# Kernel optimization log

Hardware: AMD Instinct MI355X
Metric: run time of the kernel (lower is better)

The kernel has to match this reference:

```python
import jax, jax.numpy as jnp
import numpy as np

EPS = 1e-16

def setup_inputs() -> dict:
    B, N, M, D = 32, 16384, 128, 1024
    L = 3 * M + 6  # write_lengths sum: k(M), beta(1), g(1), s(3), gamma(1), e(M), a(M)
    ks = jax.random.split(jax.random.key(0), 5)
    embeddings = jax.random.normal(ks[0], (B, D), jnp.float32)
    w_prev = jax.random.uniform(ks[1], (B, N), jnp.float32)
    w_prev = w_prev / jnp.sum(w_prev, axis=1, keepdims=True)  # valid address distribution
    mem = jax.random.normal(ks[2], (B, N, M), jnp.float32) * 0.05
    # Dense params: variance_scaling(1.4, fan_avg, uniform) ~ U(-lim, lim)
    lim = float(np.sqrt(3.0 * 1.4 / ((D + L) / 2.0)))
    W = jax.random.uniform(ks[3], (D, L), jnp.float32, -lim, lim)
    b = jax.random.normal(ks[4], (L,), jnp.float32) * 0.01
    return {"embeddings": embeddings, "w_prev": w_prev, "mem": mem, "W": W, "b": b}

def _forward(embeddings, w_prev, mem, W, b):
    M = mem.shape[-1]
    o = embeddings @ W + b  # [B, 3M+6]
    k = o[:, :M]
    beta = jax.nn.softplus(o[:, M:M + 1])
    g = jax.nn.sigmoid(o[:, M + 1:M + 2])
    s = jax.nn.softmax(o[:, M + 2:M + 5], axis=1)  # 3-tap shift
    gamma = 1.0 + jax.nn.softplus(o[:, M + 5:M + 6])
    e = jax.nn.sigmoid(o[:, M + 6:2 * M + 6])
    a = o[:, 2 * M + 6:]
    # content addressing: cosine similarity -> softmax(beta * sim)
    sim = jnp.einsum('bnm,bm->bn', mem, k) / (
        jnp.linalg.norm(mem, axis=-1) * jnp.linalg.norm(k, axis=-1, keepdims=True) + EPS)
    w_c = jax.nn.softmax(beta * sim, axis=1)
    # interpolation with previous weights
    w_g = g * w_c + (1.0 - g) * w_prev
    # circular convolution with 3-tap shift kernel s = [s(-1), s(0), s(+1)]
    w_t = (s[:, 0:1] * jnp.roll(w_g, 1, axis=1)
           + s[:, 1:2] * w_g
           + s[:, 2:3] * jnp.roll(w_g, -1, axis=1))
    # sharpening
    w_sh = w_t ** gamma
    w = w_sh / (jnp.sum(w_sh, axis=1, keepdims=True) + EPS)
    # erase + add write: mem' = mem * (1 - w e^T) + w a^T
    we = w[:, :, None] * e[:, None, :]  # [B, N, M]
    wa = w[:, :, None] * a[:, None, :]
    new_mem = mem * (1.0 - we) + wa
    return w, new_mem

def reference(embeddings, w_prev, mem, W, b):
    return _forward(embeddings, w_prev, mem, W, b)
```

## Files before the change

### kernel.cpp

```cpp
#include <hip/hip_runtime.h>
#include <math.h>

#define B 32
#define N 16384
#define M 128
#define D 1024
#define L 390
#define EPSF 1e-16f

#define O_OFF  0
#define P_OFF  (B*L)
#define S1_OFF (P_OFF + B*8)
#define S2_OFF (S1_OFF + B)
#define Z_OFF  (S2_OFF + B)

__device__ __forceinline__ float softplusf(float x) {
    return x > 20.f ? x : log1pf(expf(x));
}
__device__ __forceinline__ float sigmoidf(float x) {
    return 1.f / (1.f + expf(-x));
}

__global__ __launch_bounds__(256) void k1_gemm(const float* __restrict__ emb,
                                               const float* __restrict__ W,
                                               const float* __restrict__ bias,
                                               float* __restrict__ ws) {
    __shared__ float embS[D];
    __shared__ float red[4][64];
    const int l0 = blockIdx.x * 64;
    const int b  = blockIdx.y;
    const int t  = threadIdx.x;
    for (int i = t; i < D; i += 256) embS[i] = emb[b * D + i];
    __syncthreads();
    const int li = t & 63;
    const int q  = t >> 6;
    const int l  = l0 + li;
    float partial = 0.f;
    if (l < L) {
        const float* wp = W + (size_t)(q * 256) * L + l;
        #pragma unroll 4
        for (int d = 0; d < 256; ++d) partial += embS[q * 256 + d] * wp[(size_t)d * L];
    }
    red[q][li] = partial;
    __syncthreads();
    if (t < 64 && l0 + t < L) {
        float o = red[0][t] + red[1][t] + red[2][t] + red[3][t] + bias[l0 + t];
        ws[O_OFF + b * L + l0 + t] = o;
    }
}

__global__ __launch_bounds__(128) void k1b_act(float* __restrict__ ws) {
    const int b = blockIdx.x;
    const int t = threadIdx.x;
    const float* o = ws + O_OFF + b * L;
    float kv = o[t];
    float sq = kv * kv;
    #pragma unroll
    for (int off = 32; off >= 1; off >>= 1) sq += __shfl_xor(sq, off, 64);
    __shared__ float s01[2];
    if ((t & 63) == 0) s01[t >> 6] = sq;
    __syncthreads();
    if (t == 0) {
        float knorm = sqrtf(s01[0] + s01[1]);
        float beta  = softplusf(o[M]);
        float g     = sigmoidf(o[M + 1]);
        float x0 = o[M + 2], x1 = o[M + 3], x2 = o[M + 4];
        float mx = fmaxf(x0, fmaxf(x1, x2));
        float e0 = expf(x0 - mx), e1 = expf(x1 - mx), e2 = expf(x2 - mx);
        float inv = 1.f / (e0 + e1 + e2);
        float gamma = 1.f + softplusf(o[M + 5]);
        float* p = ws + P_OFF + b * 8;
        p[0] = beta; p[1] = g; p[2] = e0 * inv; p[3] = e1 * inv; p[4] = e2 * inv;
        p[5] = gamma; p[6] = knorm;
        ws[S1_OFF + b] = 0.f;
        ws[S2_OFF + b] = 0.f;
    }
}

__global__ __launch_bounds__(256) void k2_sim(const float* __restrict__ mem,
                                              float* __restrict__ ws) {
    const int b    = blockIdx.y;
    const int n0   = blockIdx.x * 64;
    const int t    = threadIdx.x;
    const int wave = t >> 6, lane = t & 63;
    __shared__ float kS[M];
    if (t < M) kS[t] = ws[O_OFF + b * L + t];
    __syncthreads();
    const float beta  = ws[P_OFF + b * 8 + 0];
    const float knorm = ws[P_OFF + b * 8 + 6];
    float* z = ws + Z_OFF + (size_t)b * N;
    const int seg = (lane & 15) * 8;
    const float4 ka = *(const float4*)&kS[seg];
    const float4 kb = *(const float4*)&kS[seg + 4];
    float lsum = 0.f;
    #pragma unroll
    for (int it = 0; it < 4; ++it) {
        const int n = n0 + wave * 16 + it * 4 + (lane >> 4);
        const float* mp = mem + ((size_t)b * N + n) * M + seg;
        const float4 ma = *(const float4*)mp;
        const float4 mb = *(const float4*)(mp + 4);
        float dot = ma.x*ka.x + ma.y*ka.y + ma.z*ka.z + ma.w*ka.w
                  + mb.x*kb.x + mb.y*kb.y + mb.z*kb.z + mb.w*kb.w;
        float sq  = ma.x*ma.x + ma.y*ma.y + ma.z*ma.z + ma.w*ma.w
                  + mb.x*mb.x + mb.y*mb.y + mb.z*mb.z + mb.w*mb.w;
        #pragma unroll
        for (int off = 1; off <= 8; off <<= 1) {
            dot += __shfl_xor(dot, off, 64);
            sq  += __shfl_xor(sq,  off, 64);
        }
        if ((lane & 15) == 0) {
            const float sim = dot / (sqrtf(sq) * knorm + EPSF);
            const float zz  = beta * sim;
            z[n] = zz;
            lsum += expf(zz);
        }
    }
    lsum += __shfl_xor(lsum, 16, 64);
    lsum += __shfl_xor(lsum, 32, 64);
    __shared__ float acc[4];
    if (lane == 0) acc[wave] = lsum;
    __syncthreads();
    if (t == 0) atomicAdd(ws + S1_OFF + b, acc[0] + acc[1] + acc[2] + acc[3]);
}

__global__ __launch_bounds__(256) void k3_shsum(const float* __restrict__ w_prev,
                                                float* __restrict__ ws,
                                                float* __restrict__ out) {
    const int b = blockIdx.y;
    const int n = blockIdx.x * 256 + threadIdx.x;
    const float* p = ws + P_OFF + b * 8;
    const float g = p[1], s0 = p[2], s1 = p[3], s2 = p[4], gamma = p[5];
    const float invS1 = 1.f / ws[S1_OFF + b];
    const float* z  = ws + Z_OFF + (size_t)b * N;
    const float* wp = w_prev + (size_t)b * N;
    const int nm = (n == 0)     ? N - 1 : n - 1;
    const int np = (n == N - 1) ? 0     : n + 1;
    const float gm1 = 1.f - g;
    const float wgm = g * expf(z[nm]) * invS1 + gm1 * wp[nm];
    const float wg0 = g * expf(z[n ]) * invS1 + gm1 * wp[n ];
    const float wgp = g * expf(z[np]) * invS1 + gm1 * wp[np];
    const float wt  = s0 * wgm + s1 * wg0 + s2 * wgp;
    const float v = powf(wt, gamma);
    out[(size_t)b * N + n] = v;
    float r = v;
    #pragma unroll
    for (int off = 32; off >= 1; off >>= 1) r += __shfl_xor(r, off, 64);
    __shared__ float acc[4];
    if ((threadIdx.x & 63) == 0) acc[threadIdx.x >> 6] = r;
    __syncthreads();
    if (threadIdx.x == 0) atomicAdd(ws + S2_OFF + b, acc[0] + acc[1] + acc[2] + acc[3]);
}

__global__ __launch_bounds__(256) void k4_write(const float* __restrict__ mem,
                                                const float* __restrict__ ws,
                                                float* __restrict__ out) {
    const int b    = blockIdx.y;
    const int n0   = blockIdx.x * 64;
    const int t    = threadIdx.x;
    const int wave = t >> 6, lane = t & 63;
    __shared__ float eS[M], aS[M];
    if (t < M) {
        eS[t] = sigmoidf(ws[O_OFF + b * L + M + 6 + t]);
        aS[t] = ws[O_OFF + b * L + 2 * M + 6 + t];
    }
    __syncthreads();
    const float invS2 = 1.f / (ws[S2_OFF + b] + EPSF);
    float* w_out = out + (size_t)b * N;
    float* m_out = out + (size_t)B * N;
    const int col = (lane & 31) * 4;
    const float4 ev = *(const float4*)&eS[col];
    const float4 av = *(const float4*)&aS[col];
    #pragma unroll
    for (int it = 0; it < 8; ++it) {
        const int n = n0 + wave * 16 + it * 2 + (lane >> 5);
        const float wsh = w_out[n];
        const float wv  = wsh * invS2;
        const size_t idx = ((size_t)b * N + n) * M + col;
        const float4 mv = *(const float4*)(mem + idx);
        float4 r;
        r.x = fmaf(mv.x, fmaf(-wv, ev.x, 1.f), wv * av.x);
        r.y = fmaf(mv.y, fmaf(-wv, ev.y, 1.f), wv * av.y);
        r.z = fmaf(mv.z, fmaf(-wv, ev.z, 1.f), wv * av.z);
        r.w = fmaf(mv.w, fmaf(-wv, ev.w, 1.f), wv * av.w);
        *(float4*)(m_out + idx) = r;
        if ((lane & 31) == 0) w_out[n] = wv;
    }
}

extern "C" void kernel_launch(void* const* d_in, const int* in_sizes, int n_in,
                              void* d_out, int out_size, void* d_ws, size_t ws_size,
                              hipStream_t stream) {
    const float* emb    = (const float*)d_in[0];
    const float* w_prev = (const float*)d_in[1];
    const float* mem    = (const float*)d_in[2];
    const float* W      = (const float*)d_in[3];
    const float* bias   = (const float*)d_in[4];
    float* ws  = (float*)d_ws;
    float* out = (float*)d_out;

    k1_gemm <<<dim3(7, B),      256, 0, stream>>>(emb, W, bias, ws);
    k1b_act <<<dim3(B),         128, 0, stream>>>(ws);
    k2_sim  <<<dim3(N / 64, B), 256, 0, stream>>>(mem, ws);
    k3_shsum<<<dim3(N / 256, B),256, 0, stream>>>(w_prev, ws, out);
    k4_write<<<dim3(N / 64, B), 256, 0, stream>>>(mem, ws, out);
}
```

Before: 572.2 us.

## Cache exp in sim pass, reverse write-kernel block order, use nontemporal stores

The similarity kernel now stores exp(beta*sim) directly, so the shift kernel reads precomputed values instead of recomputing three exps per element. The write kernel walks blocks in reverse order, so the tail of mem read last by the similarity kernel is read first while it may still be in cache. Its output stores become nontemporal to reduce cache pollution. The GEMM unroll factor is also raised. Storing unnormalised exp values could overflow for large beta*sim, though beta*sim is bounded by beta here.

```diff
diff --git a/kernel.cpp b/kernel.cpp
--- a/kernel.cpp
+++ b/kernel.cpp
@@ -13,6 +13,8 @@
 #define S1_OFF (P_OFF + B*8)
 #define S2_OFF (S1_OFF + B)
 #define Z_OFF  (S2_OFF + B)
+
+typedef float fvec4 __attribute__((ext_vector_type(4)));
 
 __device__ __forceinline__ float softplusf(float x) {
     return x > 20.f ? x : log1pf(expf(x));
@@ -38,7 +40,7 @@
     float partial = 0.f;
     if (l < L) {
         const float* wp = W + (size_t)(q * 256) * L + l;
-        #pragma unroll 4
+        #pragma unroll 8
         for (int d = 0; d < 256; ++d) partial += embS[q * 256 + d] * wp[(size_t)d * L];
     }
     red[q][li] = partial;
@@ -110,9 +112,9 @@
         }
         if ((lane & 15) == 0) {
             const float sim = dot / (sqrtf(sq) * knorm + EPSF);
-            const float zz  = beta * sim;
-            z[n] = zz;
-            lsum += expf(zz);
+            const float u   = expf(beta * sim);
+            z[n] = u;
+            lsum += u;
         }
     }
     lsum += __shfl_xor(lsum, 16, 64);
@@ -131,14 +133,15 @@
     const float* p = ws + P_OFF + b * 8;
     const float g = p[1], s0 = p[2], s1 = p[3], s2 = p[4], gamma = p[5];
     const float invS1 = 1.f / ws[S1_OFF + b];
-    const float* z  = ws + Z_OFF + (size_t)b * N;
+    const float* u  = ws + Z_OFF + (size_t)b * N;
     const float* wp = w_prev + (size_t)b * N;
     const int nm = (n == 0)     ? N - 1 : n - 1;
     const int np = (n == N - 1) ? 0     : n + 1;
     const float gm1 = 1.f - g;
-    const float wgm = g * expf(z[nm]) * invS1 + gm1 * wp[nm];
-    const float wg0 = g * expf(z[n ]) * invS1 + gm1 * wp[n ];
-    const float wgp = g * expf(z[np]) * invS1 + gm1 * wp[np];
+    const float gi  = g * invS1;
+    const float wgm = gi * u[nm] + gm1 * wp[nm];
+    const float wg0 = gi * u[n ] + gm1 * wp[n ];
+    const float wgp = gi * u[np] + gm1 * wp[np];
     const float wt  = s0 * wgm + s1 * wg0 + s2 * wgp;
     const float v = powf(wt, gamma);
     out[(size_t)b * N + n] = v;
@@ -155,7 +158,7 @@
                                                 const float* __restrict__ ws,
                                                 float* __restrict__ out) {
     const int b    = blockIdx.y;
-    const int n0   = blockIdx.x * 64;
+    const int n0   = (gridDim.x - 1 - blockIdx.x) * 64;
     const int t    = threadIdx.x;
     const int wave = t >> 6, lane = t & 63;
     __shared__ float eS[M], aS[M];
@@ -168,22 +171,23 @@
     float* w_out = out + (size_t)b * N;
     float* m_out = out + (size_t)B * N;
     const int col = (lane & 31) * 4;
-    const float4 ev = *(const float4*)&eS[col];
-    const float4 av = *(const float4*)&aS[col];
+    const fvec4 ev = *(const fvec4*)&eS[col];
+    const fvec4 av = *(const fvec4*)&aS[col];
     #pragma unroll
     for (int it = 0; it < 8; ++it) {
         const int n = n0 + wave * 16 + it * 2 + (lane >> 5);
         const float wsh = w_out[n];
         const float wv  = wsh * invS2;
         const size_t idx = ((size_t)b * N + n) * M + col;
-        const float4 mv = *(const float4*)(mem + idx);
-        float4 r;
+        const fvec4 mv = *(const fvec4*)(mem + idx);
+        fvec4 r;
         r.x = fmaf(mv.x, fmaf(-wv, ev.x, 1.f), wv * av.x);
         r.y = fmaf(mv.y, fmaf(-wv, ev.y, 1.f), wv * av.y);
         r.z = fmaf(mv.z, fmaf(-wv, ev.z, 1.f), wv * av.z);
         r.w = fmaf(mv.w, fmaf(-wv, ev.w, 1.f), wv * av.w);
-        *(float4*)(m_out + idx) = r;
-        if ((lane & 31) == 0) w_out[n] = wv;
+        __builtin_nontemporal_store(r, (fvec4*)(m_out + idx));
+        if ((lane & 31) == 0)
+            __builtin_nontemporal_store(wv, w_out + n);
     }
 }
 
```

Result: no change. 561.7 us (-1.8%).
